# Kernel tuning notes

Measured on AMD Instinct MI355X. Metric: run time of the kernel, lower is better.

## Reference

```python
import jax, jax.numpy as jnp
import numpy as np


def _lstm_cell(x, h, c, w_ih, w_hh, b_ih, b_hh):
    # PyTorch gate order: i, f, g, o ; w_ih: [4H,E], w_hh: [4H,H]
    gates = x @ w_ih.T + b_ih + h @ w_hh.T + b_hh  # [B,4H]
    H = h.shape[-1]
    i, f, g, o = jnp.split(gates, 4, axis=-1)
    c_new = jax.nn.sigmoid(f) * c + jax.nn.sigmoid(i) * jnp.tanh(g)
    h_new = jax.nn.sigmoid(o) * jnp.tanh(c_new)
    return h_new, c_new


def setup_inputs() -> dict:
    key = jax.random.key(0)
    ks = jax.random.split(key, 16)
    V, E, B, S_ENC, S_DEC = 32000, 512, 16, 512, 128
    s = 0.02
    return {
        "encode_input": jax.random.randint(ks[0], (B, S_ENC), 0, V),
        "decode_input": jax.random.randint(ks[1], (B, S_DEC), 0, V),
        "embedding": jax.random.normal(ks[2], (V, E), jnp.float32) * s,
        "w_ih_e": jax.random.normal(ks[3], (4 * E, E), jnp.float32) * s,
        "w_hh_e": jax.random.normal(ks[4], (4 * E, E), jnp.float32) * s,
        "b_ih_e": jax.random.normal(ks[5], (4 * E,), jnp.float32) * s,
        "b_hh_e": jax.random.normal(ks[6], (4 * E,), jnp.float32) * s,
        "w_ih_d": jax.random.normal(ks[7], (4 * E, E), jnp.float32) * s,
        "w_hh_d": jax.random.normal(ks[8], (4 * E, E), jnp.float32) * s,
        "b_ih_d": jax.random.normal(ks[9], (4 * E,), jnp.float32) * s,
        "b_hh_d": jax.random.normal(ks[10], (4 * E,), jnp.float32) * s,
        "w_proj": jax.random.normal(ks[11], (V, 2 * E), jnp.float32) * s,
        "b_proj": jax.random.normal(ks[12], (V,), jnp.float32) * s,
    }


def reference(encode_input, decode_input, embedding,
              w_ih_e, w_hh_e, b_ih_e, b_hh_e,
              w_ih_d, w_hh_d, b_ih_d, b_hh_d,
              w_proj, b_proj):
    B = encode_input.shape[0]
    E = embedding.shape[1]
    T_dec = decode_input.shape[1]

    # ---- encoder LSTM over full source sequence (zero initial state) ----
    enc_embeds = embedding[encode_input]  # [B,S,E]
    h0 = jnp.zeros((B, E), embedding.dtype)
    c0 = jnp.zeros((B, E), embedding.dtype)

    def enc_step(carry, x_t):
        h, c = carry
        h, c = _lstm_cell(x_t, h, c, w_ih_e, w_hh_e, b_ih_e, b_hh_e)
        return (h, c), h

    (hT, cT), enc_out_t = jax.lax.scan(enc_step, (h0, c0), jnp.swapaxes(enc_embeds, 0, 1))
    enc_out = jnp.swapaxes(enc_out_t, 0, 1)  # [B,S,E]

    # ---- decoder: self-feeding LSTM (only step-0 embedding is used) + attention ----
    dec_embeds = embedding[decode_input]  # [B,T,E]
    x0 = dec_embeds[:, 0, :]

    def dec_step(carry, _):
        x, h, c = carry
        h, c = _lstm_cell(x, h, c, w_ih_d, w_hh_d, b_ih_d, b_hh_d)
        scores = jnp.einsum('bh,bsh->bs', h, enc_out)
        attn = jax.nn.softmax(scores, axis=-1)
        ctx = jnp.einsum('bs,bsh->bh', attn, enc_out)
        return (h, h, c), (h, ctx)

    _, (hs, ctxs) = jax.lax.scan(dec_step, (x0, hT, cT), None, length=T_dec)
    dec_out = jnp.concatenate([hs, ctxs], axis=-1)       # [T,B,2E]
    dec_out = jnp.swapaxes(dec_out, 0, 1)                # [B,T,2E]

    logits = dec_out @ w_proj.T + b_proj                 # [B,T,V]
    return logits
```

## Files before the change

### kernel.cpp

```cpp
#include <hip/hip_runtime.h>
#include <hip/hip_bf16.h>
#include <stdint.h>

typedef __attribute__((ext_vector_type(4))) float f32x4;
typedef __attribute__((ext_vector_type(2))) float f32x2;
typedef __attribute__((ext_vector_type(8))) short s16x8;
typedef __attribute__((ext_vector_type(4))) uint32_t u32x4;
typedef __hip_bfloat16 bf16;
typedef unsigned long long u64;

__device__ __forceinline__ float sigf(float x){ return 1.f/(1.f+__expf(-x)); }
__device__ __forceinline__ float tanh_f(float x){ float e=__expf(2.f*x); return (e-1.f)/(e+1.f); }

__device__ __forceinline__ u64 ld_u64_agent(const u64* p){
  return __hip_atomic_load(p, __ATOMIC_RELAXED, __HIP_MEMORY_SCOPE_AGENT);
}
__device__ __forceinline__ void st_u64_agent(u64* p, u64 v){
  __hip_atomic_store(p, v, __ATOMIC_RELAXED, __HIP_MEMORY_SCOPE_AGENT);
}

__device__ __forceinline__ void gload_lds16(const void* g, void* l){
  __builtin_amdgcn_global_load_lds(
      (const __attribute__((address_space(1))) uint32_t*)g,
      (__attribute__((address_space(3))) uint32_t*)l, 16, 0, 0);
}

__global__ __launch_bounds__(256) void k_convert(const float* __restrict__ in, bf16* __restrict__ outp, int n){
  int i = (blockIdx.x*256 + threadIdx.x)*4;
  if (i >= n) return;
  f32x4 v = *(const f32x4*)&in[i];
  alignas(8) bf16 tmp[4] = {__float2bfloat16(v.x), __float2bfloat16(v.y), __float2bfloat16(v.z), __float2bfloat16(v.w)};
  *(uint64_t*)&outp[i] = *(const uint64_t*)tmp;
}

__global__ __launch_bounds__(256) void k_embed(const int* __restrict__ enc_in, const float* __restrict__ emb,
                                               bf16* __restrict__ Xe){
  int i = blockIdx.x*256 + threadIdx.x;
  int o = i*4;
  int row = o >> 9, e = o & 511;
  int t = row >> 4, b = row & 15;
  int tok = enc_in[b*512 + t];
  f32x4 v = *(const f32x4*)&emb[(size_t)tok*512 + e];
  alignas(8) bf16 tmp[4] = {__float2bfloat16(v.x), __float2bfloat16(v.y), __float2bfloat16(v.z), __float2bfloat16(v.w)};
  *(uint64_t*)&Xe[o] = *(const uint64_t*)tmp;
}

template<int OUT_BF16>
__global__ __launch_bounds__(256) void k_gemm(
    const bf16* __restrict__ A, const bf16* __restrict__ Bm,
    const float* __restrict__ bias1, const float* __restrict__ bias2,
    void* __restrict__ Cp, int M, int N, int K)
{
  __shared__ bf16 Al[128*32];
  __shared__ bf16 Bl[128*32];
  const int tid = threadIdx.x;
  const int n0 = blockIdx.x*128, m0 = blockIdx.y*128;
  const int wv = tid >> 6, lane = tid & 63;
  const int wr = (wv >> 1)*64, wc = (wv & 1)*64;
  const int lrow = lane & 15, lk = (lane >> 4)*8;
  const int r1 = tid >> 2, kq = (tid & 3)*8;

  f32x4 acc[4][4];
  #pragma unroll
  for (int i=0;i<4;++i)
    #pragma unroll
    for (int j=0;j<4;++j) { f32x4 z = {0.f,0.f,0.f,0.f}; acc[i][j] = z; }

  const bf16* pa0 = &A[(size_t)(m0 + r1)*K + kq];
  const bf16* pa1 = &A[(size_t)(m0 + 64 + r1)*K + kq];
  const bf16* pb0 = &Bm[(size_t)(n0 + r1)*K + kq];
  const bf16* pb1 = &Bm[(size_t)(n0 + 64 + r1)*K + kq];

  char* AlB = (char*)Al + wv*1024;
  char* BlB = (char*)Bl + wv*1024;

  const int nk = K >> 5;
  for (int kt = 0; kt < nk; ++kt) {
    __syncthreads();
    int off = kt*32;
    gload_lds16(pa0 + off, AlB);
    gload_lds16(pa1 + off, AlB + 4096);
    gload_lds16(pb0 + off, BlB);
    gload_lds16(pb1 + off, BlB + 4096);
    __syncthreads();
    s16x8 af[4], bfr[4];
    #pragma unroll
    for (int mi=0;mi<4;++mi) af[mi]  = *(const s16x8*)&Al[(wr + mi*16 + lrow)*32 + lk];
    #pragma unroll
    for (int ni=0;ni<4;++ni) bfr[ni] = *(const s16x8*)&Bl[(wc + ni*16 + lrow)*32 + lk];
    #pragma unroll
    for (int mi=0;mi<4;++mi)
      #pragma unroll
      for (int ni=0;ni<4;++ni)
        acc[mi][ni] = __builtin_amdgcn_mfma_f32_16x16x32_bf16(af[mi], bfr[ni], acc[mi][ni], 0, 0, 0);
  }
  const int crow = (lane >> 4)*4;
  #pragma unroll
  for (int mi=0;mi<4;++mi) {
    #pragma unroll
    for (int ni=0;ni<4;++ni) {
      int cc = n0 + wc + ni*16 + lrow;
      float badd = (bias1 ? bias1[cc] : 0.f) + (bias2 ? bias2[cc] : 0.f);
      #pragma unroll
      for (int q=0;q<4;++q) {
        int rr = m0 + wr + mi*16 + crow + q;
        float v = acc[mi][ni][q] + badd;
        if (OUT_BF16) ((bf16*)Cp)[(size_t)rr*N + cc] = __float2bfloat16(v);
        else          ((float*)Cp)[(size_t)rr*N + cc] = v;
      }
    }
  }
}


__global__ __launch_bounds__(512, 1) void k_enc_r(
    const bf16* __restrict__ GXe, const float* __restrict__ w_hh,
    u64* __restrict__ hex, float* __restrict__ cT, float* __restrict__ hT,
    float* __restrict__ enc_out)
{
  const int tid = threadIdx.x, bid = blockIdx.x;
  const int b = bid >> 4, r = bid & 15;
  const int ksl = tid & 15, c = tid >> 4;

  __shared__ float h_lds[512];
  __shared__ float gate_lds[128];

  f32x4 wreg[4][8];
  #pragma unroll
  for (int cc = 0; cc < 4; ++cc) {
    int ic = c*4 + cc;
    int gc = (ic >> 5)*512 + r*32 + (ic & 31);
    const float* wrow = &w_hh[(size_t)gc*512 + ksl*32];
    #pragma unroll
    for (int i = 0; i < 8; ++i) wreg[cc][i] = *(const f32x4*)&wrow[((i + ksl) & 7)*4];
  }
  const int gc0 = ((c*4) >> 5)*512 + r*32 + ((c*4) & 31);
  u64* hb = hex + (size_t)b*1024;
  float c_reg = 0.f;
  const int jg = r*32 + tid;

  for (int t = 0; t < 512; ++t) {
    uint64_t gx = 0;
    if (ksl == 0) gx = *(const uint64_t*)&GXe[(size_t)(t*16 + b)*2048 + gc0];
    float a0=0.f, a1=0.f, a2=0.f, a3=0.f;
    if (t > 0) {
      const uint32_t tg = (uint32_t)t;
      u64* slot = &hb[(t & 1)*512 + tid];
      u64 v = ld_u64_agent(slot);
      uint32_t spins = 0;
      while ((uint32_t)(v >> 32) != tg) {
        v = ld_u64_agent(slot);
        if (++spins > (1u<<18)) break;
      }
      h_lds[tid] = __uint_as_float((uint32_t)v);
      __syncthreads();
      const float* hrow = &h_lds[ksl*32];
      #pragma unroll
      for (int i = 0; i < 8; ++i) {
        f32x4 hv = *(const f32x4*)&hrow[((i + ksl) & 7)*4];
        a0 = __fmaf_rn(hv.x, wreg[0][i].x, a0); a0 = __fmaf_rn(hv.y, wreg[0][i].y, a0);
        a0 = __fmaf_rn(hv.z, wreg[0][i].z, a0); a0 = __fmaf_rn(hv.w, wreg[0][i].w, a0);
        a1 = __fmaf_rn(hv.x, wreg[1][i].x, a1); a1 = __fmaf_rn(hv.y, wreg[1][i].y, a1);
        a1 = __fmaf_rn(hv.z, wreg[1][i].z, a1); a1 = __fmaf_rn(hv.w, wreg[1][i].w, a1);
        a2 = __fmaf_rn(hv.x, wreg[2][i].x, a2); a2 = __fmaf_rn(hv.y, wreg[2][i].y, a2);
        a2 = __fmaf_rn(hv.z, wreg[2][i].z, a2); a2 = __fmaf_rn(hv.w, wreg[2][i].w, a2);
        a3 = __fmaf_rn(hv.x, wreg[3][i].x, a3); a3 = __fmaf_rn(hv.y, wreg[3][i].y, a3);
        a3 = __fmaf_rn(hv.z, wreg[3][i].z, a3); a3 = __fmaf_rn(hv.w, wreg[3][i].w, a3);
      }
      #pragma unroll
      for (int s = 1; s < 16; s <<= 1) {
        a0 += __shfl_xor(a0, s); a1 += __shfl_xor(a1, s);
        a2 += __shfl_xor(a2, s); a3 += __shfl_xor(a3, s);
      }
    }
    if (ksl == 0) {
      gate_lds[c*4 + 0] = a0 + __uint_as_float((uint32_t)(gx & 0xffffu) << 16);
      gate_lds[c*4 + 1] = a1 + __uint_as_float((uint32_t)((gx >> 16) & 0xffffu) << 16);
      gate_lds[c*4 + 2] = a2 + __uint_as_float((uint32_t)((gx >> 32) & 0xffffu) << 16);
      gate_lds[c*4 + 3] = a3 + __uint_as_float((uint32_t)((gx >> 48) & 0xffffu) << 16);
    }
    __syncthreads();
    if (tid < 32) {
      float gi = gate_lds[tid];
      float gf = gate_lds[32 + tid];
      float gg = gate_lds[64 + tid];
      float go = gate_lds[96 + tid];
      float cn = sigf(gf)*c_reg + sigf(gi)*tanh_f(gg);
      float hn = sigf(go)*tanh_f(cn);
      c_reg = cn;
      st_u64_agent(&hb[((t+1) & 1)*512 + jg],
                   ((u64)(uint32_t)(t + 1) << 32) | (u64)__float_as_uint(hn));
      enc_out[((size_t)b*512 + t)*512 + jg] = hn;
      if (t == 511) { hT[b*512 + jg] = hn; cT[b*512 + jg] = cn; }
    }
  }
}

__global__ __launch_bounds__(128) void k_gates0(
    const int* __restrict__ dec_in, const float* __restrict__ emb,
    const float* __restrict__ hT,
    const float* __restrict__ w_ih, const float* __restrict__ w_hh,
    const float* __restrict__ b_ih, const float* __restrict__ b_hh,
    float* __restrict__ g0)
{
  int gt = blockIdx.x*128 + threadIdx.x;
  int b = gt & 15, col = gt >> 4;
  const float* x0 = &emb[(size_t)dec_in[b*128] * 512];
  const float* hp = &hT[b*512];
  const float* wi = &w_ih[(size_t)col*512];
  const float* wh = &w_hh[(size_t)col*512];
  float s0=0.f, s1=0.f;
  for (int k = 0; k < 512; k += 4) {
    f32x4 xv = *(const f32x4*)&x0[k]; f32x4 wv = *(const f32x4*)&wi[k];
    f32x4 hv = *(const f32x4*)&hp[k]; f32x4 w2 = *(const f32x4*)&wh[k];
    s0 += xv.x*wv.x + xv.y*wv.y + xv.z*wv.z + xv.w*wv.w;
    s1 += hv.x*w2.x + hv.y*w2.y + hv.z*w2.z + hv.w*w2.w;
  }
  g0[b*2048 + col] = s0 + s1 + b_ih[col] + b_hh[col];
}

__global__ __launch_bounds__(512, 1) void k_dec_r(
    const float* __restrict__ w_ih, const float* __restrict__ w_hh,
    const float* __restrict__ b_ih, const float* __restrict__ b_hh,
    const float* __restrict__ gates0,
    u64* __restrict__ hex, const float* __restrict__ cT,
    float* __restrict__ dec_h, bf16* __restrict__ dec_out)
{
  const int tid = threadIdx.x, bid = blockIdx.x;
  const int b = bid >> 4, r = bid & 15;
  const int ksl = tid & 15, c = tid >> 4;

  __shared__ float h_lds[512];
  __shared__ float gate_lds[128];

  f32x4 wreg[4][8];
  float bias_c[4];
  #pragma unroll
  for (int cc = 0; cc < 4; ++cc) {
    int ic = c*4 + cc;
    int gc = (ic >> 5)*512 + r*32 + (ic & 31);
    bias_c[cc] = b_ih[gc] + b_hh[gc];
    const float* wra = &w_ih[(size_t)gc*512 + ksl*32];
    const float* wrb = &w_hh[(size_t)gc*512 + ksl*32];
    #pragma unroll
    for (int i = 0; i < 8; ++i) {
      int o = ((i + ksl) & 7)*4;
      f32x4 wa = *(const f32x4*)&wra[o];
      f32x4 wb = *(const f32x4*)&wrb[o];
      wreg[cc][i] = wa + wb;
    }
  }
  const int gc0 = ((c*4) >> 5)*512 + r*32 + ((c*4) & 31);
  u64* hb = hex + (size_t)b*1024;
  const int jg = r*32 + tid;
  float c_reg = 0.f;
  if (tid < 32) c_reg = cT[b*512 + jg];

  for (int t = 0; t < 128; ++t) {
    float a0=0.f, a1=0.f, a2=0.f, a3=0.f;
    if (t > 0) {
      const uint32_t tg = (uint32_t)t;
      u64* slot = &hb[(t & 1)*512 + tid];
      u64 v = ld_u64_agent(slot);
      uint32_t spins = 0;
      while ((uint32_t)(v >> 32) != tg) {
        v = ld_u64_agent(slot);
        if (++spins > (1u<<18)) break;
      }
      h_lds[tid] = __uint_as_float((uint32_t)v);
      __syncthreads();
      const float* hrow = &h_lds[ksl*32];
      #pragma unroll
      for (int i = 0; i < 8; ++i) {
        f32x4 hv = *(const f32x4*)&hrow[((i + ksl) & 7)*4];
        a0 = __fmaf_rn(hv.x, wreg[0][i].x, a0); a0 = __fmaf_rn(hv.y, wreg[0][i].y, a0);
        a0 = __fmaf_rn(hv.z, wreg[0][i].z, a0); a0 = __fmaf_rn(hv.w, wreg[0][i].w, a0);
        a1 = __fmaf_rn(hv.x, wreg[1][i].x, a1); a1 = __fmaf_rn(hv.y, wreg[1][i].y, a1);
        a1 = __fmaf_rn(hv.z, wreg[1][i].z, a1); a1 = __fmaf_rn(hv.w, wreg[1][i].w, a1);
        a2 = __fmaf_rn(hv.x, wreg[2][i].x, a2); a2 = __fmaf_rn(hv.y, wreg[2][i].y, a2);
        a2 = __fmaf_rn(hv.z, wreg[2][i].z, a2); a2 = __fmaf_rn(hv.w, wreg[2][i].w, a2);
        a3 = __fmaf_rn(hv.x, wreg[3][i].x, a3); a3 = __fmaf_rn(hv.y, wreg[3][i].y, a3);
        a3 = __fmaf_rn(hv.z, wreg[3][i].z, a3); a3 = __fmaf_rn(hv.w, wreg[3][i].w, a3);
      }
      #pragma unroll
      for (int s = 1; s < 16; s <<= 1) {
        a0 += __shfl_xor(a0, s); a1 += __shfl_xor(a1, s);
        a2 += __shfl_xor(a2, s); a3 += __shfl_xor(a3, s);
      }
    }
    if (ksl == 0) {
      if (t == 0) {
        f32x4 gv = *(const f32x4*)&gates0[(size_t)b*2048 + gc0];
        gate_lds[c*4 + 0] = gv.x; gate_lds[c*4 + 1] = gv.y;
        gate_lds[c*4 + 2] = gv.z; gate_lds[c*4 + 3] = gv.w;
      } else {
        gate_lds[c*4 + 0] = a0 + bias_c[0];
        gate_lds[c*4 + 1] = a1 + bias_c[1];
        gate_lds[c*4 + 2] = a2 + bias_c[2];
        gate_lds[c*4 + 3] = a3 + bias_c[3];
      }
    }
    __syncthreads();
    if (tid < 32) {
      float gi = gate_lds[tid];
      float gf = gate_lds[32 + tid];
      float gg = gate_lds[64 + tid];
      float go = gate_lds[96 + tid];
      float cn = sigf(gf)*c_reg + sigf(gi)*tanh_f(gg);
      float hn = sigf(go)*tanh_f(cn);
      c_reg = cn;
      st_u64_agent(&hb[((t+1) & 1)*512 + jg],
                   ((u64)(uint32_t)(t + 1) << 32) | (u64)__float_as_uint(hn));
      dec_h[((size_t)t*16 + b)*512 + jg] = hn;
      dec_out[((size_t)(b*128 + t))*1024 + jg] = __float2bfloat16(hn);
    }
  }
}

__global__ __launch_bounds__(256) void k_attn(
    const float* __restrict__ dec_h, const float* __restrict__ enc_out,
    bf16* __restrict__ dOut)
{
  const int tid = threadIdx.x, bid = blockIdx.x;
  const int b = bid >> 3, t0 = (bid & 7)*16;
  __shared__ float h16[16*512];
  __shared__ float sc[16*512];
  #pragma unroll
  for (int q = 0; q < 8; ++q) {
    int fi = q*256 + tid;
    int tt = fi >> 7, e4 = (fi & 127)*4;
    *(f32x4*)&h16[tt*512 + e4] = *(const f32x4*)&dec_h[((size_t)(t0 + tt)*16 + b)*512 + e4];
  }
  __syncthreads();
  const float* encb = &enc_out[(size_t)b*512*512];
  for (int si = 0; si < 2; ++si) {
    int s = si*256 + tid;
    float a[16];
    #pragma unroll
    for (int tt=0;tt<16;++tt) a[tt]=0.f;
    for (int e4 = 0; e4 < 512; e4 += 4) {
      f32x4 ev = *(const f32x4*)&encb[(size_t)s*512 + e4];
      #pragma unroll
      for (int tt = 0; tt < 16; ++tt) {
        f32x4 hv = *(const f32x4*)&h16[tt*512 + e4];
        a[tt] += ev.x*hv.x + ev.y*hv.y + ev.z*hv.z + ev.w*hv.w;
      }
    }
    #pragma unroll
    for (int tt=0;tt<16;++tt) sc[tt*512 + s] = a[tt];
  }
  __syncthreads();
  {
    int wv = tid >> 6, lane = tid & 63;
    #pragma unroll
    for (int u = 0; u < 4; ++u) {
      int tt = wv*4 + u;
      float x[8];
      float m = -1e30f;
      #pragma unroll
      for (int i=0;i<8;++i){ x[i] = sc[tt*512 + i*64 + lane]; m = fmaxf(m, x[i]); }
      #pragma unroll
      for (int off=1; off<64; off<<=1) m = fmaxf(m, __shfl_xor(m, off));
      float sum = 0.f;
      #pragma unroll
      for (int i=0;i<8;++i){ x[i] = __expf(x[i]-m); sum += x[i]; }
      #pragma unroll
      for (int off=1; off<64; off<<=1) sum += __shfl_xor(sum, off);
      float inv = 1.f/sum;
      #pragma unroll
      for (int i=0;i<8;++i) sc[tt*512 + i*64 + lane] = x[i]*inv;
    }
  }
  __syncthreads();
  {
    int e0 = tid*2;
    float cx[16], cy[16];
    #pragma unroll
    for (int tt=0;tt<16;++tt){ cx[tt]=0.f; cy[tt]=0.f; }
    for (int s = 0; s < 512; ++s) {
      f32x2 ev = *(const f32x2*)&encb[(size_t)s*512 + e0];
      #pragma unroll
      for (int tt = 0; tt < 16; ++tt) {
        float aw = sc[tt*512 + s];
        cx[tt] += aw*ev.x; cy[tt] += aw*ev.y;
      }
    }
    #pragma unroll
    for (int tt = 0; tt < 16; ++tt) {
      size_t rowo = ((size_t)(b*128 + t0 + tt))*1024 + 512 + e0;
      alignas(4) bf16 tmp[2] = {__float2bfloat16(cx[tt]), __float2bfloat16(cy[tt])};
      *(uint32_t*)&dOut[rowo] = *(const uint32_t*)tmp;
    }
  }
}

extern "C" void kernel_launch(void* const* d_in, const int* in_sizes, int n_in,
                              void* d_out, int out_size, void* d_ws, size_t ws_size,
                              hipStream_t stream)
{
  const int*   enc_in = (const int*)d_in[0];
  const int*   dec_in = (const int*)d_in[1];
  const float* emb    = (const float*)d_in[2];
  const float* w_ih_e = (const float*)d_in[3];
  const float* w_hh_e = (const float*)d_in[4];
  const float* b_ih_e = (const float*)d_in[5];
  const float* b_hh_e = (const float*)d_in[6];
  const float* w_ih_d = (const float*)d_in[7];
  const float* w_hh_d = (const float*)d_in[8];
  const float* b_ih_d = (const float*)d_in[9];
  const float* b_hh_d = (const float*)d_in[10];
  const float* w_proj = (const float*)d_in[11];
  const float* b_proj = (const float*)d_in[12];
  float* out = (float*)d_out;

  char* ws = (char*)d_ws;
  size_t off = 0;
  auto alloc = [&](size_t bytes)->void* { void* p = ws + off; off += (bytes + 255) & ~(size_t)255; return p; };
  bf16*  Wp      = (bf16*)alloc(32000ull*1024*2);
  bf16*  Xe      = (bf16*)alloc(8192ull*512*2);
  bf16*  Wie     = (bf16*)alloc(2048ull*512*2);
  bf16*  GXe     = (bf16*)alloc(8192ull*2048*2);
  float* enc_out = (float*)alloc(16ull*512*512*4);
  float* dec_h   = (float*)alloc(128ull*16*512*4);
  bf16*  dOutB   = (bf16*)alloc(2048ull*1024*2);
  u64*   hexE    = (u64*)alloc(16ull*1024*8);
  u64*   hexD    = (u64*)alloc(16ull*1024*8);
  float* cT      = (float*)alloc(16*512*4);
  float* hT      = (float*)alloc(16*512*4);
  float* g0      = (float*)alloc(16*2048*4);
  if (off > ws_size) return;

  (void)hipMemsetAsync(hexE, 0, 16ull*1024*8*2, stream);

  k_convert<<<32000, 256, 0, stream>>>(w_proj, Wp, 32768000);
  k_convert<<<1024, 256, 0, stream>>>(w_ih_e, Wie, 1048576);
  k_embed<<<4096, 256, 0, stream>>>(enc_in, emb, Xe);
  k_gemm<1><<<dim3(16, 64), 256, 0, stream>>>(Xe, Wie, b_ih_e, b_hh_e, GXe, 8192, 2048, 512);
  k_enc_r<<<256, 512, 0, stream>>>(GXe, w_hh_e, hexE, cT, hT, enc_out);
  k_gates0<<<256, 128, 0, stream>>>(dec_in, emb, hT, w_ih_d, w_hh_d, b_ih_d, b_hh_d, g0);
  k_dec_r<<<256, 512, 0, stream>>>(w_ih_d, w_hh_d, b_ih_d, b_hh_d, g0, hexD, cT, dec_h, dOutB);
  k_attn<<<128, 256, 0, stream>>>(dec_h, enc_out, dOutB);
  k_gemm<0><<<dim3(250, 16), 256, 0, stream>>>(dOutB, Wp, b_proj, nullptr, out, 2048, 32000, 1024);
}
```

Before: 1.733 ms.

## Map each gate column group to one hidden unit, dropping gate LDS exchange

Remaps the encoder and decoder recurrent kernels so each 16-lane group computes all four gates (i, f, g, o) for a single hidden unit, instead of four consecutive gate columns. The cell update can then run directly in the ksl==0 lanes, with no gate_lds staging buffer and no second __syncthreads per timestep. This targets per-step latency on the serial recurrence. In exchange, the input-gate loads become four strided scalar bf16 loads instead of one packed 64-bit load. With a single barrier per step left guarding h_lds, there is also a possible reuse race on h_lds between consecutive steps.

Result: slower. 1.778 ms (+2.6%).

```diff
diff --git a/kernel.cpp b/kernel.cpp
--- a/kernel.cpp
+++ b/kernel.cpp
@@ -121,27 +121,29 @@
   const int tid = threadIdx.x, bid = blockIdx.x;
   const int b = bid >> 4, r = bid & 15;
   const int ksl = tid & 15, c = tid >> 4;
+  const int jg = r*32 + c;
 
   __shared__ float h_lds[512];
-  __shared__ float gate_lds[128];
 
   f32x4 wreg[4][8];
   #pragma unroll
-  for (int cc = 0; cc < 4; ++cc) {
-    int ic = c*4 + cc;
-    int gc = (ic >> 5)*512 + r*32 + (ic & 31);
-    const float* wrow = &w_hh[(size_t)gc*512 + ksl*32];
-    #pragma unroll
-    for (int i = 0; i < 8; ++i) wreg[cc][i] = *(const f32x4*)&wrow[((i + ksl) & 7)*4];
-  }
-  const int gc0 = ((c*4) >> 5)*512 + r*32 + ((c*4) & 31);
+  for (int g = 0; g < 4; ++g) {
+    const float* wrow = &w_hh[(size_t)(g*512 + jg)*512 + ksl*32];
+    #pragma unroll
+    for (int i = 0; i < 8; ++i) wreg[g][i] = *(const f32x4*)&wrow[((i + ksl) & 7)*4];
+  }
   u64* hb = hex + (size_t)b*1024;
   float c_reg = 0.f;
-  const int jg = r*32 + tid;
 
   for (int t = 0; t < 512; ++t) {
-    uint64_t gx = 0;
-    if (ksl == 0) gx = *(const uint64_t*)&GXe[(size_t)(t*16 + b)*2048 + gc0];
+    float gx0=0.f, gx1=0.f, gx2=0.f, gx3=0.f;
+    if (ksl == 0) {
+      const bf16* gp = &GXe[(size_t)(t*16 + b)*2048 + jg];
+      gx0 = __bfloat162float(gp[0]);
+      gx1 = __bfloat162float(gp[512]);
+      gx2 = __bfloat162float(gp[1024]);
+      gx3 = __bfloat162float(gp[1536]);
+    }
     float a0=0.f, a1=0.f, a2=0.f, a3=0.f;
     if (t > 0) {
       const uint32_t tg = (uint32_t)t;
@@ -174,17 +176,7 @@
       }
     }
     if (ksl == 0) {
-      gate_lds[c*4 + 0] = a0 + __uint_as_float((uint32_t)(gx & 0xffffu) << 16);
-      gate_lds[c*4 + 1] = a1 + __uint_as_float((uint32_t)((gx >> 16) & 0xffffu) << 16);
-      gate_lds[c*4 + 2] = a2 + __uint_as_float((uint32_t)((gx >> 32) & 0xffffu) << 16);
-      gate_lds[c*4 + 3] = a3 + __uint_as_float((uint32_t)((gx >> 48) & 0xffffu) << 16);
-    }
-    __syncthreads();
-    if (tid < 32) {
-      float gi = gate_lds[tid];
-      float gf = gate_lds[32 + tid];
-      float gg = gate_lds[64 + tid];
-      float go = gate_lds[96 + tid];
+      float gi = a0 + gx0, gf = a1 + gx1, gg = a2 + gx2, go = a3 + gx3;
       float cn = sigf(gf)*c_reg + sigf(gi)*tanh_f(gg);
       float hn = sigf(go)*tanh_f(cn);
       c_reg = cn;
@@ -229,17 +221,16 @@
   const int tid = threadIdx.x, bid = blockIdx.x;
   const int b = bid >> 4, r = bid & 15;
   const int ksl = tid & 15, c = tid >> 4;
+  const int jg = r*32 + c;
 
   __shared__ float h_lds[512];
-  __shared__ float gate_lds[128];
 
   f32x4 wreg[4][8];
-  float bias_c[4];
+  float bias_g[4];
   #pragma unroll
-  for (int cc = 0; cc < 4; ++cc) {
-    int ic = c*4 + cc;
-    int gc = (ic >> 5)*512 + r*32 + (ic & 31);
-    bias_c[cc] = b_ih[gc] + b_hh[gc];
+  for (int g = 0; g < 4; ++g) {
+    int gc = g*512 + jg;
+    bias_g[g] = b_ih[gc] + b_hh[gc];
     const float* wra = &w_ih[(size_t)gc*512 + ksl*32];
     const float* wrb = &w_hh[(size_t)gc*512 + ksl*32];
     #pragma unroll
@@ -247,14 +238,12 @@
       int o = ((i + ksl) & 7)*4;
       f32x4 wa = *(const f32x4*)&wra[o];
       f32x4 wb = *(const f32x4*)&wrb[o];
-      wreg[cc][i] = wa + wb;
-    }
-  }
-  const int gc0 = ((c*4) >> 5)*512 + r*32 + ((c*4) & 31);
+      wreg[g][i] = wa + wb;
+    }
+  }
   u64* hb = hex + (size_t)b*1024;
-  const int jg = r*32 + tid;
   float c_reg = 0.f;
-  if (tid < 32) c_reg = cT[b*512 + jg];
+  if (ksl == 0) c_reg = cT[b*512 + jg];
 
   for (int t = 0; t < 128; ++t) {
     float a0=0.f, a1=0.f, a2=0.f, a3=0.f;
@@ -289,23 +278,14 @@
       }
     }
     if (ksl == 0) {
+      float gi, gf, gg, go;
       if (t == 0) {
-        f32x4 gv = *(const f32x4*)&gates0[(size_t)b*2048 + gc0];
-        gate_lds[c*4 + 0] = gv.x; gate_lds[c*4 + 1] = gv.y;
-        gate_lds[c*4 + 2] = gv.z; gate_lds[c*4 + 3] = gv.w;
+        const float* gp = &gates0[(size_t)b*2048 + jg];
+        gi = gp[0]; gf = gp[512]; gg = gp[1024]; go = gp[1536];
       } else {
-        gate_lds[c*4 + 0] = a0 + bias_c[0];
-        gate_lds[c*4 + 1] = a1 + bias_c[1];
-        gate_lds[c*4 + 2] = a2 + bias_c[2];
-        gate_lds[c*4 + 3] = a3 + bias_c[3];
-      }
-    }
-    __syncthreads();
-    if (tid < 32) {
-      float gi = gate_lds[tid];
-      float gf = gate_lds[32 + tid];
-      float gg = gate_lds[64 + tid];
-      float go = gate_lds[96 + tid];
+        gi = a0 + bias_g[0]; gf = a1 + bias_g[1];
+        gg = a2 + bias_g[2]; go = a3 + bias_g[3];
+      }
       float cn = sigf(gf)*c_reg + sigf(gi)*tanh_f(gg);
       float hn = sigf(go)*tanh_f(cn);
       c_reg = cn;
```
